# Kernel tuning notes

Measured on AMD Instinct MI355X. Metric: run time of the kernel, lower is better.

The kernel has to match this reference:

```python
import jax, jax.numpy as jnp
import numpy as np
from math import comb

# --- module hyperparameters (from init_kwargs / module-level constants) ---
F = 32          # features
NITER = 3       # num_iterations
NB = 16         # num_basis_functions
NDCM = 4        # n_dcm
CUTOFF = 4.0
MAXZ = 17       # max_atomic_number
NC = 9          # (max_degree+1)^2 spherical components, max_degree=2
DEG = np.array([0, 1, 1, 1, 2, 2, 2, 2, 2])  # degree l of each component
BINOM = jnp.asarray([comb(NB - 1, k) for k in range(NB)], dtype=jnp.float32)


def _np_sph9(x, y, z):
    # real spherical harmonics up to l=2 on the unit sphere (numpy, for Gaunt table)
    c0 = 0.28209479177387814; c1 = 0.4886025119029199
    c2a = 1.0925484305920792; c2b = 0.31539156525252005; c2c = 0.5462742152960396
    return np.stack([c0 * np.ones_like(x), c1 * y, c1 * z, c1 * x,
                     c2a * x * y, c2a * y * z, c2b * (3.0 * z * z - 1.0),
                     c2a * x * z, c2c * (x * x - y * y)], axis=0)


def _gaunt():
    # real Gaunt (Clebsch-Gordan-type) coefficients G[a,b,c] = int Y_a Y_b Y_c dOmega
    # via Gauss-Legendre (cos theta) x midpoint (phi) quadrature -- exact for l<=2 products
    ct, wt = np.polynomial.legendre.leggauss(64)
    nph = 256
    phi = (np.arange(nph) + 0.5) * (2.0 * np.pi / nph)
    st = np.sqrt(1.0 - ct ** 2)
    x = st[:, None] * np.cos(phi)[None, :]
    y = st[:, None] * np.sin(phi)[None, :]
    z = np.broadcast_to(ct[:, None], x.shape)
    w = (wt[:, None] * (2.0 * np.pi / nph)) * np.ones((1, nph))
    Y = _np_sph9(x, y, z)
    G = np.einsum('aij,bij,cij,ij->abc', Y, Y, Y, w)
    G[np.abs(G) < 1e-6] = 0.0
    return G

CG = jnp.asarray(_gaunt(), dtype=jnp.float32)  # (9, 9, 9), sparse


def _sph9(u):
    # u: (E, 3) unit vectors -> (E, 9)
    x, y, z = u[:, 0], u[:, 1], u[:, 2]
    c0 = 0.28209479177387814; c1 = 0.4886025119029199
    c2a = 1.0925484305920792; c2b = 0.31539156525252005; c2c = 0.5462742152960396
    return jnp.stack([jnp.full_like(x, c0), c1 * y, c1 * z, c1 * x,
                      c2a * x * y, c2a * y * z, c2b * (3.0 * z * z - 1.0),
                      c2a * x * z, c2c * (x * x - y * y)], axis=-1)


def _radial(r):
    # reciprocal Bernstein radial basis * smooth cutoff; r: (E,) -> (E, NB)
    u = 1.0 / (1.0 + r)
    k = jnp.arange(NB, dtype=jnp.float32)
    rb = BINOM * u[:, None] ** k * (1.0 - u[:, None]) ** (NB - 1 - k)
    t = r / CUTOFF
    den = jnp.where(t < 1.0, 1.0 - t * t, 1.0)
    fc = jnp.where(t < 1.0, jnp.exp(-t * t / den), 0.0)  # smooth_cutoff
    return rb * fc[:, None]


def _equiv_dense(x, W, b=None):
    # per-degree linear (equivariant Dense): x (N, 9, Fin), W (3, Fin, Fout); bias on l=0 only
    y = jnp.einsum('ncf,cfg->ncg', x, W[DEG])
    if b is not None:
        y = y.at[:, 0, :].add(b)
    return y


def _tp(xs, bf):
    # Gaunt tensor-product contraction: out[e,c,f] = sum_ab CG[a,b,c] xs[e,a,f] bf[e,b,f]
    # loop over the 9 fixed output components to avoid an (E,9,9,F) intermediate
    out = []
    for c in range(NC):
        t = jnp.einsum('eaf,ab->ebf', xs, CG[:, :, c])
        out.append(jnp.sum(t * bf, axis=1))
    return jnp.stack(out, axis=1)


def _forward(atomic_numbers, positions, dst_idx, src_idx, embed, Wb, W1, b1, W2, b2,
             Wt00, Wt11, Wmono, element_bias):
    n = atomic_numbers.shape[0]
    disp = positions[src_idx] - positions[dst_idx]                 # (E, 3) gather
    r = jnp.sqrt(jnp.sum(disp * disp, axis=-1) + 1e-12)            # safe norm
    u = disp / r[:, None]
    basis = _sph9(u)[:, :, None] * _radial(r)[:, None, :]          # (E, 9, NB)
    x = jnp.zeros((n, NC, F), dtype=positions.dtype).at[:, 0, :].set(embed[atomic_numbers])
    for i in range(NITER):  # message passing iterations
        bf = jnp.einsum('ebn,bng->ebg', basis, Wb[i][DEG])         # per-degree radial->feature mix (E,9,F)
        msg = _tp(x[src_idx], bf)                                  # gather src + tensor product
        y = x + jax.ops.segment_sum(msg, dst_idx, num_segments=n)  # scatter-aggregate + residual add
        y = _equiv_dense(y, W1[i], b1[i])
        y = jax.nn.silu(y)
        y = _equiv_dense(y, W2[i], b2[i])
        x = x + y                                                  # residual update
    # TensorDense to n_dcm channels, then readout heads
    mono = (x[:, 0, :] @ Wt00) @ Wmono + element_bias[atomic_numbers][:, None]  # (N, NDCM)
    dip = jnp.einsum('ncf,fg->ncg', x[:, 1:4, :], Wt11)            # (N, 3, NDCM) vector channel
    dip = jnp.clip(jax.nn.silu(dip), -0.3, 0.3) + positions[:, :, None]
    return mono, dip


def setup_inputs():
    key = jax.random.key(0)
    ks = jax.random.split(key, 12)
    N, E = 10000, 160000
    return {
        'atomic_numbers': jax.random.randint(ks[0], (N,), 0, MAXZ + 1),
        'positions': jax.random.normal(ks[1], (N, 3), jnp.float32) * 3.0,
        'dst_idx': jax.random.randint(ks[2], (E,), 0, N),
        'src_idx': jax.random.randint(ks[3], (E,), 0, N),
        'embed': jax.random.normal(ks[4], (MAXZ + 1, F), jnp.float32),
        'Wb': jax.random.normal(ks[5], (NITER, 3, NB, F), jnp.float32) / np.sqrt(NB).astype(np.float32),
        'W1': jax.random.normal(ks[6], (NITER, 3, F, F), jnp.float32) / np.sqrt(F).astype(np.float32),
        'b1': jnp.zeros((NITER, F), jnp.float32),
        'W2': jax.random.normal(ks[7], (NITER, 3, F, F), jnp.float32) / np.sqrt(F).astype(np.float32),
        'b2': jnp.zeros((NITER, F), jnp.float32),
        'Wt00': jax.random.normal(ks[8], (F, NDCM), jnp.float32) / np.sqrt(F).astype(np.float32),
        'Wt11': jax.random.normal(ks[9], (F, NDCM), jnp.float32) / np.sqrt(F).astype(np.float32),
        'Wmono': jax.random.normal(ks[10], (NDCM, NDCM), jnp.float32) / np.sqrt(NDCM).astype(np.float32),
        'element_bias': jnp.zeros((MAXZ + 1,), jnp.float32),
    }


def reference(atomic_numbers, positions, dst_idx, src_idx, embed, Wb, W1, b1, W2, b2,
              Wt00, Wt11, Wmono, element_bias):
    return _forward(atomic_numbers, positions, dst_idx, src_idx, embed, Wb, W1, b1, W2, b2,
                    Wt00, Wt11, Wmono, element_bias)
```

## Files before the change

kernel.cpp:

```cpp
#include <hip/hip_runtime.h>
#include <hip/hip_bf16.h>


#define NITER 3
#define BCAP  64

#define OFF_WB    0
#define OFF_W1    4608
#define OFF_B1    13824
#define OFF_W2    13920
#define OFF_B2    23136
#define OFF_WT00  23232
#define OFF_WT11  23360
#define OFF_WMONO 23488
#define OFF_EB    23504
#define OFF_EMB   23522
#define WC_TOTAL  24098

__device__ __forceinline__ float b2f(const __hip_bfloat16 v) { return __bfloat162float(v); }

#define KC0 0.28209479177387814f
#define KG1 0.21850968611841584f
#define KG2 0.12615662610100802f
#define KG3 0.18022375157287861f
#define KG4 0.09011187578643931f
#define KG5 0.15607834722743988f

__device__ __forceinline__ float ldany(const void* p, int i, bool f32) {
    return f32 ? ((const float*)p)[i] : b2f(((const __hip_bfloat16*)p)[i]);
}

__device__ __forceinline__ bool wave_sniff(const void* pos) {
    const __hip_bfloat16* p = (const __hip_bfloat16*)pos;
    int lane = threadIdx.x & 63;
    int bad = 0;
    #pragma unroll
    for (int k = 0; k < 4; k++) {
        float v = b2f(p[lane + k*64]);
        bad |= !(fabsf(v) < 1.0e6f);
    }
    return __ballot(bad) != 0ull;
}

__device__ __forceinline__ float xadd32(float v) {
    return v + __int_as_float(__shfl_xor(__float_as_int(v), 32, 64));
}

__device__ __forceinline__ bool edge_geom(float dx, float dy, float dz,
                                          float* sp, float* rad) {
    float r2 = dx*dx + dy*dy + dz*dz + 1e-12f;
    if (r2 >= 16.0f) return false;
    float r  = sqrtf(r2);
    float t2 = r2 * 0.0625f;
    float fc = __expf(-t2 / (1.0f - t2));
    float u = 1.0f / (1.0f + r);
    float v = 1.0f - u;
    const float BIN[16] = {1.f,15.f,105.f,455.f,1365.f,3003.f,5005.f,6435.f,
                           6435.f,5005.f,3003.f,1365.f,455.f,105.f,15.f,1.f};
    float vp[16];
    vp[0] = 1.0f;
    #pragma unroll
    for (int k = 1; k < 16; k++) vp[k] = vp[k-1] * v;
    float up = 1.0f;
    #pragma unroll
    for (int n = 0; n < 16; n++) { rad[n] = BIN[n] * up * vp[15-n] * fc; up *= u; }
    float ir = 1.0f / r;
    float ux = dx*ir, uy = dy*ir, uz = dz*ir;
    const float c0 = 0.28209479177387814f, c1 = 0.4886025119029199f;
    const float c2a = 1.0925484305920792f, c2b = 0.31539156525252005f, c2c = 0.5462742152960396f;
    sp[0] = c0;
    sp[1] = c1*uy; sp[2] = c1*uz; sp[3] = c1*ux;
    sp[4] = c2a*ux*uy; sp[5] = c2a*uy*uz; sp[6] = c2b*(3.0f*uz*uz - 1.0f);
    sp[7] = c2a*ux*uz; sp[8] = c2c*(ux*ux - uy*uy);
    return true;
}

__device__ __forceinline__ void write_geo_slot(float* gp,
                                               const float* sp, const float* rad) {
    float4* g4 = (float4*)gp;
    g4[0] = make_float4(sp[0], sp[1], sp[2], sp[3]);
    g4[1] = make_float4(sp[4], sp[5], sp[6], sp[7]);
    g4[2] = make_float4(sp[8], 0.f, 0.f, 0.f);
    g4[4] = make_float4(rad[0],  rad[1],  rad[2],  rad[3]);
    g4[5] = make_float4(rad[4],  rad[5],  rad[6],  rad[7]);
    g4[6] = make_float4(rad[8],  rad[9],  rad[10], rad[11]);
    g4[7] = make_float4(rad[12], rad[13], rad[14], rad[15]);
}

template <bool FIRST, bool LAST>
__global__ __launch_bounds__(256, 4) void iter_kernel(
        const float* __restrict__ xin, float* __restrict__ xout,
        const float* __restrict__ geo2, const int* __restrict__ cur,
        const int* __restrict__ sidx,
        const float* __restrict__ Wbi,
        const float* __restrict__ W1i, const float* __restrict__ b1i,
        const float* __restrict__ W2i, const float* __restrict__ b2i,
        const int* __restrict__ an, const float* __restrict__ posf,
        const float* __restrict__ wc, const void* __restrict__ pos,
        void* __restrict__ out_, int N) {
    constexpr int NCH = LAST ? 4 : 9;
    constexpr int NR  = LAST ? 2 : 5;
    __shared__ float sw[1536];
    __shared__ float sm[4][12][33];
    bool f32o = false;
    if (LAST) f32o = wave_sniff(pos);
    int tid   = threadIdx.x;
    int wslot = tid >> 6;
    int lane  = tid & 63;
    int f     = lane & 31;
    int half  = lane >> 5;
    int n     = blockIdx.x * 4 + wslot;
    bool act  = (n < N);
    float (*tile)[33] = sm[wslot];

    for (int i = tid; i < 1536; i += 256) sw[i] = Wbi[i];
    __syncthreads();

    float A0=0.f,A1=0.f,A2=0.f,A3=0.f,A4=0.f,A5=0.f,A6=0.f,A7=0.f,A8=0.f;
    if (act) {
        int cnt = __builtin_amdgcn_readfirstlane(cur[n]);
        int h0c = (cnt + 1) >> 1;
        int beg = n * BCAP;
        int b0  = beg + (half ? h0c : 0);
        int b1e = beg + (half ? cnt : h0c);
        int e = b0;
        int s_cur = (e < b1e) ? sidx[e] : 0;
        while (e < b1e) {
            int s_nxt = (e + 1 < b1e) ? sidx[e + 1] : 0;
            float X0, X1, X2, X3, X4, X5, X6, X7, X8;
            if (FIRST) {
                X0 = xin[(size_t)s_cur * 32 + f];
                X1=X2=X3=X4=X5=X6=X7=X8=0.f;
            } else {
                const float* xp = xin + (size_t)s_cur * 384 + f * 12;
                float4 xa = *(const float4*)(xp);
                float4 xb = *(const float4*)(xp + 4);
                X8 = xp[8];
                X0=xa.x; X1=xa.y; X2=xa.z; X3=xa.w;
                X4=xb.x; X5=xb.y; X6=xb.z; X7=xb.w;
            }
            const float4* gp = (const float4*)(geo2 + (size_t)e * 32);
            float4 h0 = gp[0], h1 = gp[1], h2 = gp[2];
            float4 r0 = gp[4], r1 = gp[5], r2 = gp[6], r3 = gp[7];
            float rad[16] = {r0.x,r0.y,r0.z,r0.w, r1.x,r1.y,r1.z,r1.w,
                             r2.x,r2.y,r2.z,r2.w, r3.x,r3.y,r3.z,r3.w};
            float rw0 = 0.f, rw1 = 0.f, rw2 = 0.f;
            #pragma unroll
            for (int k = 0; k < 16; k++) {
                rw0 = fmaf(rad[k], sw[       k*32 + f], rw0);
                rw1 = fmaf(rad[k], sw[ 512 + k*32 + f], rw1);
                rw2 = fmaf(rad[k], sw[1024 + k*32 + f], rw2);
            }
            float B0 = h0.x*rw0;
            float B1 = h0.y*rw1, B2 = h0.z*rw1, B3 = h0.w*rw1;
            float B4 = h1.x*rw2, B5 = h1.y*rw2, B6 = h1.z*rw2,
                  B7 = h1.w*rw2, B8 = h2.x*rw2;
            if (FIRST) {
                float k0 = KC0 * X0;
                A0 += k0*B0; A1 += k0*B1; A2 += k0*B2; A3 += k0*B3; A4 += k0*B4;
                A5 += k0*B5; A6 += k0*B6; A7 += k0*B7; A8 += k0*B8;
            } else {
                A0 += KC0*(X0*B0 + X1*B1 + X2*B2 + X3*B3 + X4*B4 + X5*B5 + X6*B6 + X7*B7 + X8*B8);
                A1 += KC0*(X0*B1 + X1*B0) + KG1*(X3*B4 + X4*B3 + X2*B5 + X5*B2)
                    - KG2*(X1*B6 + X6*B1) - KG1*(X1*B8 + X8*B1);
                A2 += KC0*(X0*B2 + X2*B0) + KG1*(X1*B5 + X5*B1 + X3*B7 + X7*B3)
                    + 2.0f*KG2*(X2*B6 + X6*B2);
                A3 += KC0*(X0*B3 + X3*B0) + KG1*(X1*B4 + X4*B1 + X2*B7 + X7*B2)
                    - KG2*(X3*B6 + X6*B3) + KG1*(X3*B8 + X8*B3);
                if (!LAST) {
                    A4 += KC0*(X0*B4 + X4*B0) + KG1*(X1*B3 + X3*B1) + KG5*(X5*B7 + X7*B5)
                        - KG3*(X4*B6 + X6*B4);
                    A5 += KC0*(X0*B5 + X5*B0) + KG1*(X1*B2 + X2*B1) + KG5*(X4*B7 + X7*B4)
                        + KG4*(X5*B6 + X6*B5) - KG5*(X5*B8 + X8*B5);
                    A6 += KC0*(X0*B6 + X6*B0) - KG2*X1*B1 + 2.0f*KG2*X2*B2 - KG2*X3*B3
                        - KG3*X4*B4 + KG4*X5*B5 + KG3*X6*B6 + KG4*X7*B7 - KG3*X8*B8;
                    A7 += KC0*(X0*B7 + X7*B0) + KG1*(X2*B3 + X3*B2) + KG5*(X4*B5 + X5*B4)
                        + KG4*(X6*B7 + X7*B6) + KG5*(X7*B8 + X8*B7);
                    A8 += KC0*(X0*B8 + X8*B0) - KG1*X1*B1 + KG1*X3*B3 - KG5*X5*B5 + KG5*X7*B7
                        - KG3*(X6*B8 + X8*B6);
                }
            }
            s_cur = s_nxt; e++;
        }
    }
    A0 = xadd32(A0); A1 = xadd32(A1); A2 = xadd32(A2); A3 = xadd32(A3);
    if (!LAST) {
        A4 = xadd32(A4); A5 = xadd32(A5); A6 = xadd32(A6);
        A7 = xadd32(A7); A8 = xadd32(A8);
    }

    float xr[9];
    #pragma unroll
    for (int c = 0; c < 9; c++) xr[c] = 0.f;
    if (act) {
        if (FIRST) {
            xr[0] = xin[(size_t)n * 32 + f];
        } else {
            const float* xp = xin + (size_t)n * 384 + f * 12;
            float4 xa = *(const float4*)(xp);
            float4 xb = *(const float4*)(xp + 4);
            xr[0]=xa.x; xr[1]=xa.y; xr[2]=xa.z; xr[3]=xa.w;
            xr[4]=xb.x; xr[5]=xb.y; xr[6]=xb.z; xr[7]=xb.w;
            xr[8]=xp[8];
        }
    }

    if (act && half == 0) {
        tile[0][f] = xr[0] + A0;
        tile[1][f] = xr[1] + A1;
        tile[2][f] = xr[2] + A2;
        tile[3][f] = xr[3] + A3;
        if (!LAST) {
            tile[4][f] = xr[4] + A4;
            tile[5][f] = xr[5] + A5;
            tile[6][f] = xr[6] + A6;
            tile[7][f] = xr[7] + A7;
            tile[8][f] = xr[8] + A8;
        }
    }
    __syncthreads();

    int g = f;
    float o1[NR];
    #pragma unroll
    for (int cc = 0; cc < NR; cc++) {
        int c  = cc*2 + half;
        int cs = (c < NCH) ? c : 0;
        int d  = (cs == 0) ? 0 : ((cs < 4) ? 1 : 2);
        const float* W1p = W1i + d * 1024;
        float acc = (c == 0) ? b1i[g] : 0.f;
        #pragma unroll
        for (int fi = 0; fi < 32; fi++)
            acc = fmaf(tile[cs][fi], W1p[fi*32 + g], acc);
        acc = acc * __builtin_amdgcn_rcpf(1.0f + __expf(-acc));
        o1[cc] = acc;
    }
    __syncthreads();
    #pragma unroll
    for (int cc = 0; cc < NR; cc++) {
        int c = cc*2 + half;
        if (c < NCH) tile[c][g] = o1[cc];
    }
    __syncthreads();

    float xf[NR];
    #pragma unroll
    for (int cc = 0; cc < NR; cc++) {
        int c  = cc*2 + half;
        int cs = (c < NCH) ? c : 0;
        int d  = (cs == 0) ? 0 : ((cs < 4) ? 1 : 2);
        const float* W2p = W2i + d * 1024;
        float acc = (c == 0) ? b2i[g] : 0.f;
        #pragma unroll
        for (int fi = 0; fi < 32; fi++)
            acc = fmaf(tile[cs][fi], W2p[fi*32 + g], acc);
        xf[cc] = xr[cs] + acc;
        if (LAST && act) {
            const float* WT = (c == 0) ? (wc + OFF_WT00) : (wc + OFF_WT11);
            float v0 = xf[cc] * WT[g*4 + 0];
            float v1 = xf[cc] * WT[g*4 + 1];
            float v2 = xf[cc] * WT[g*4 + 2];
            float v3 = xf[cc] * WT[g*4 + 3];
            #pragma unroll
            for (int m = 1; m <= 16; m <<= 1) {
                v0 += __shfl_xor(v0, m, 64);
                v1 += __shfl_xor(v1, m, 64);
                v2 += __shfl_xor(v2, m, 64);
                v3 += __shfl_xor(v3, m, 64);
            }
            if (g == 0) {
                if (c == 0) {
                    const float* Wmono = wc + OFF_WMONO;
                    float ebv = wc[OFF_EB + an[n]];
                    #pragma unroll
                    for (int m = 0; m < 4; m++) {
                        float a2 = ebv + v0*Wmono[0*4+m] + v1*Wmono[1*4+m]
                                       + v2*Wmono[2*4+m] + v3*Wmono[3*4+m];
                        if (f32o) ((float*)out_)[n*4 + m] = a2;
                        else ((__hip_bfloat16*)out_)[n*4 + m] = __float2bfloat16(a2);
                    }
                } else {
                    float pc = posf[n*3 + (c - 1)];
                    float pv[4] = {v0, v1, v2, v3};
                    #pragma unroll
                    for (int m = 0; m < 4; m++) {
                        float v = pv[m];
                        v = v * __builtin_amdgcn_rcpf(1.0f + __expf(-v));
                        v = fminf(fmaxf(v, -0.3f), 0.3f);
                        v += pc;
                        size_t o = (size_t)N*4 + (size_t)n*12 + (size_t)(c-1)*4 + m;
                        if (f32o) ((float*)out_)[o] = v;
                        else ((__hip_bfloat16*)out_)[o] = __float2bfloat16(v);
                    }
                }
            }
        }
    }
    if (!LAST) {
        __syncthreads();
        #pragma unroll
        for (int cc = 0; cc < NR; cc++) {
            int c = cc*2 + half;
            if (c < 9) tile[c][g] = xf[cc];
        }
        if (half == 1) { tile[9][g] = 0.f; tile[10][g] = 0.f; tile[11][g] = 0.f; }
        __syncthreads();
        if (act) {
            float* xo = xout + (size_t)n * 384;
            *(float4*)(xo + f*12 + half*4) =
                make_float4(tile[half*4+0][f], tile[half*4+1][f],
                            tile[half*4+2][f], tile[half*4+3][f]);
            if (half == 0)
                *(float4*)(xo + f*12 + 8) =
                    make_float4(tile[8][f], tile[9][f], tile[10][f], tile[11][f]);
        }
    }
}

__global__ void setup_kernel(const void* pos, const void* Wb, const void* W1,
        const void* b1, const void* W2, const void* b2, const void* Wt00,
        const void* Wt11, const void* Wmono, const void* eb, const void* emb,
        const int* __restrict__ an,
        const int* __restrict__ srcI, const int* __restrict__ dstI,
        float* __restrict__ posf, float* __restrict__ wc,
        float* __restrict__ x, float* __restrict__ geo2, int* __restrict__ cur,
        int* __restrict__ sidx, int N, int E, int use_csr) {
    bool f32 = wave_sniff(pos);
    int i = blockIdx.x * blockDim.x + threadIdx.x;
    int np = N * 3;
    if (i < np) { posf[i] = ldany(pos, i, f32); return; }
    int j = i - np;
    if (j < WC_TOTAL) {
        const void* src; int rel;
        if      (j < OFF_W1)    { src = Wb;    rel = j; }
        else if (j < OFF_B1)    { src = W1;    rel = j - OFF_W1; }
        else if (j < OFF_W2)    { src = b1;    rel = j - OFF_B1; }
        else if (j < OFF_B2)    { src = W2;    rel = j - OFF_W2; }
        else if (j < OFF_WT00)  { src = b2;    rel = j - OFF_B2; }
        else if (j < OFF_WT11)  { src = Wt00;  rel = j - OFF_WT00; }
        else if (j < OFF_WMONO) { src = Wt11;  rel = j - OFF_WT11; }
        else if (j < OFF_EB)    { src = Wmono; rel = j - OFF_WMONO; }
        else if (j < OFF_EMB)   { src = eb;    rel = j - OFF_EB; }
        else                    { src = emb;   rel = j - OFF_EMB; }
        wc[j] = ldany(src, rel, f32);
        return;
    }
    j -= WC_TOTAL;
    if (j < N * 32) {
        int n = j >> 5, rem = j & 31;
        size_t o = use_csr ? ((size_t)n * 32 + rem)
                           : ((size_t)n * 288 + rem);
        x[o] = ldany(emb, an[n] * 32 + rem, f32);
        return;
    }
    j -= N * 32;
    if (j < E && use_csr) {
        int s = srcI[j], d = dstI[j];
        float sp[9], rad[16];
        if (!edge_geom(ldany(pos, s*3+0, f32) - ldany(pos, d*3+0, f32),
                       ldany(pos, s*3+1, f32) - ldany(pos, d*3+1, f32),
                       ldany(pos, s*3+2, f32) - ldany(pos, d*3+2, f32),
                       sp, rad)) return;
        int slot = atomicAdd(&cur[d], 1);
        sidx[d * BCAP + slot] = s;
        write_geo_slot(geo2 + ((size_t)d * BCAP + slot) * 32, sp, rad);
    }
}

__global__ void zero_kernel(float4* __restrict__ b, int n) {
    int i = blockIdx.x * blockDim.x + threadIdx.x;
    int stride = gridDim.x * blockDim.x;
    float4 z = make_float4(0.f, 0.f, 0.f, 0.f);
    for (; i < n; i += stride) b[i] = z;
}

__global__ __launch_bounds__(256) void edge_inline_kernel(
        const float* __restrict__ x, float* __restrict__ y,
        const float* __restrict__ posf,
        const int* __restrict__ srcI, const int* __restrict__ dstI,
        const float* __restrict__ Wbi, int E) {
    int f  = threadIdx.x & 31;
    int hw = (blockIdx.x * blockDim.x + threadIdx.x) >> 5;
    int nhw = gridDim.x * (blockDim.x >> 5);
    float w0[16], w1[16], w2[16];
    #pragma unroll
    for (int n = 0; n < 16; n++) {
        w0[n] = Wbi[(0*16 + n)*32 + f];
        w1[n] = Wbi[(1*16 + n)*32 + f];
        w2[n] = Wbi[(2*16 + n)*32 + f];
    }
    for (int e = hw; e < E; e += nhw) {
        int s = srcI[e], d = dstI[e];
        float sp[9], rad[16];
        if (!edge_geom(posf[s*3+0] - posf[d*3+0],
                       posf[s*3+1] - posf[d*3+1],
                       posf[s*3+2] - posf[d*3+2], sp, rad)) continue;
        float rw0 = 0.f, rw1 = 0.f, rw2 = 0.f;
        #pragma unroll
        for (int n = 0; n < 16; n++) {
            rw0 = fmaf(rad[n], w0[n], rw0);
            rw1 = fmaf(rad[n], w1[n], rw1);
            rw2 = fmaf(rad[n], w2[n], rw2);
        }
        float B0 = sp[0]*rw0;
        float B1 = sp[1]*rw1, B2 = sp[2]*rw1, B3 = sp[3]*rw1;
        float B4 = sp[4]*rw2, B5 = sp[5]*rw2, B6 = sp[6]*rw2,
              B7 = sp[7]*rw2, B8 = sp[8]*rw2;
        const float* xp = x + (size_t)s*288 + f;
        float X0 = xp[0],   X1 = xp[32],  X2 = xp[64],  X3 = xp[96],  X4 = xp[128];
        float X5 = xp[160], X6 = xp[192], X7 = xp[224], X8 = xp[256];
        float* yp = y + (size_t)d*288 + f;
        float m;
        m = KC0*(X0*B0 + X1*B1 + X2*B2 + X3*B3 + X4*B4 + X5*B5 + X6*B6 + X7*B7 + X8*B8);
        unsafeAtomicAdd(yp + 0, m);
        m = KC0*(X0*B1 + X1*B0) + KG1*(X3*B4 + X4*B3 + X2*B5 + X5*B2)
          - KG2*(X1*B6 + X6*B1) - KG1*(X1*B8 + X8*B1);
        unsafeAtomicAdd(yp + 32, m);
        m = KC0*(X0*B2 + X2*B0) + KG1*(X1*B5 + X5*B1 + X3*B7 + X7*B3)
          + 2.0f*KG2*(X2*B6 + X6*B2);
        unsafeAtomicAdd(yp + 64, m);
        m = KC0*(X0*B3 + X3*B0) + KG1*(X1*B4 + X4*B1 + X2*B7 + X7*B2)
          - KG2*(X3*B6 + X6*B3) + KG1*(X3*B8 + X8*B3);
        unsafeAtomicAdd(yp + 96, m);
        m = KC0*(X0*B4 + X4*B0) + KG1*(X1*B3 + X3*B1) + KG5*(X5*B7 + X7*B5)
          - KG3*(X4*B6 + X6*B4);
        unsafeAtomicAdd(yp + 128, m);
        m = KC0*(X0*B5 + X5*B0) + KG1*(X1*B2 + X2*B1) + KG5*(X4*B7 + X7*B4)
          + KG4*(X5*B6 + X6*B5) - KG5*(X5*B8 + X8*B5);
        unsafeAtomicAdd(yp + 160, m);
        m = KC0*(X0*B6 + X6*B0) - KG2*X1*B1 + 2.0f*KG2*X2*B2 - KG2*X3*B3
          - KG3*X4*B4 + KG4*X5*B5 + KG3*X6*B6 + KG4*X7*B7 - KG3*X8*B8;
        unsafeAtomicAdd(yp + 192, m);
        m = KC0*(X0*B7 + X7*B0) + KG1*(X2*B3 + X3*B2) + KG5*(X4*B5 + X5*B4)
          + KG4*(X6*B7 + X7*B6) + KG5*(X7*B8 + X8*B7);
        unsafeAtomicAdd(yp + 224, m);
        m = KC0*(X0*B8 + X8*B0) - KG1*X1*B1 + KG1*X3*B3 - KG5*X5*B5 + KG5*X7*B7
          - KG3*(X6*B8 + X8*B6);
        unsafeAtomicAdd(yp + 256, m);
    }
}

__global__ __launch_bounds__(256) void atom_kernel(
        float* __restrict__ x, const float* __restrict__ y,
        const float* __restrict__ W1i, const float* __restrict__ b1i,
        const float* __restrict__ W2i, const float* __restrict__ b2i,
        int N) {
    __shared__ float sm[4][64*33];
    int lane  = threadIdx.x & 63;
    int wslot = threadIdx.x >> 6;
    int u = __builtin_amdgcn_readfirstlane(blockIdx.x * 4 + wslot);
    int t = u / 9;
    int c = u - t * 9;
    int d = (c == 0) ? 0 : ((c < 4) ? 1 : 2);
    const float* W1 = W1i + d * 1024;
    const float* W2 = W2i + d * 1024;
    float* tile = sm[wslot];
    float4 xr4[8];
    #pragma unroll
    for (int k = 0; k < 8; k++) {
        int e  = lane * 4 + k * 256;
        int al = e >> 5, f = e & 31;
        int ag = t * 64 + al;
        float4 s = make_float4(0.f, 0.f, 0.f, 0.f);
        float4 xv = make_float4(0.f, 0.f, 0.f, 0.f);
        if (ag < N) {
            xv = *(const float4*)(x + (size_t)ag * 288 + c * 32 + f);
            float4 yv = *(const float4*)(y + (size_t)ag * 288 + c * 32 + f);
            s = make_float4(xv.x + yv.x, xv.y + yv.y, xv.z + yv.z, xv.w + yv.w);
        }
        xr4[k] = xv;
        *(float4*)(tile + al * 33 + f) = s;
    }
    __syncthreads();
    float yin[32];
    #pragma unroll
    for (int k = 0; k < 8; k++) {
        float4 v = *(const float4*)(tile + lane * 33 + 4 * k);
        yin[4*k+0] = v.x; yin[4*k+1] = v.y; yin[4*k+2] = v.z; yin[4*k+3] = v.w;
    }
    float acc[32];
    #pragma unroll
    for (int g = 0; g < 32; g++) acc[g] = (c == 0) ? b1i[g] : 0.0f;
    #pragma unroll 4
    for (int fi = 0; fi < 32; fi++) {
        float v = yin[fi];
        #pragma unroll
        for (int g = 0; g < 32; g++) acc[g] = fmaf(v, W1[fi*32 + g], acc[g]);
    }
    #pragma unroll
    for (int g = 0; g < 32; g++)
        acc[g] = acc[g] * __builtin_amdgcn_rcpf(1.0f + __expf(-acc[g]));
    float out[32];
    #pragma unroll
    for (int g = 0; g < 32; g++) out[g] = (c == 0) ? b2i[g] : 0.0f;
    #pragma unroll 4
    for (int fi = 0; fi < 32; fi++) {
        float v = acc[fi];
        #pragma unroll
        for (int g = 0; g < 32; g++) out[g] = fmaf(v, W2[fi*32 + g], out[g]);
    }
    __syncthreads();
    #pragma unroll
    for (int k = 0; k < 8; k++)
        *(float4*)(tile + lane * 33 + 4 * k) =
            make_float4(out[4*k+0], out[4*k+1], out[4*k+2], out[4*k+3]);
    __syncthreads();
    #pragma unroll
    for (int k = 0; k < 8; k++) {
        int e  = lane * 4 + k * 256;
        int al = e >> 5, f = e & 31;
        int ag = t * 64 + al;
        if (ag < N) {
            float4 dv = *(const float4*)(tile + al * 33 + f);
            float4 xv = xr4[k];
            *(float4*)(x + (size_t)ag * 288 + c * 32 + f) =
                make_float4(xv.x + dv.x, xv.y + dv.y, xv.z + dv.z, xv.w + dv.w);
        }
    }
}

__global__ void readout_kernel(const float* __restrict__ x,
        const int* __restrict__ an, const float* __restrict__ posf,
        const float* __restrict__ wc, const void* __restrict__ pos,
        void* __restrict__ out, int N) {
    bool f32 = wave_sniff(pos);
    int n = blockIdx.x * blockDim.x + threadIdx.x;
    if (n >= N) return;
    const float* Wt00  = wc + OFF_WT00;
    const float* Wt11  = wc + OFF_WT11;
    const float* Wmono = wc + OFF_WMONO;
    const float* xb = x + (size_t)n * 288;
    float q[4] = {0.f, 0.f, 0.f, 0.f};
    for (int f = 0; f < 32; f++) {
        float xv = xb[f];
        #pragma unroll
        for (int j = 0; j < 4; j++) q[j] = fmaf(xv, Wt00[f*4 + j], q[j]);
    }
    float ebv = wc[OFF_EB + an[n]];
    #pragma unroll
    for (int m = 0; m < 4; m++) {
        float acc = ebv;
        #pragma unroll
        for (int j = 0; j < 4; j++) acc = fmaf(q[j], Wmono[j*4 + m], acc);
        if (f32) ((float*)out)[n*4 + m] = acc;
        else ((__hip_bfloat16*)out)[n*4 + m] = __float2bfloat16(acc);
    }
    #pragma unroll
    for (int c = 0; c < 3; c++) {
        float pc = posf[n*3 + c];
        const float* xc = xb + (1 + c)*32;
        float dq[4] = {0.f, 0.f, 0.f, 0.f};
        for (int f = 0; f < 32; f++) {
            float xv = xc[f];
            #pragma unroll
            for (int m = 0; m < 4; m++) dq[m] = fmaf(xv, Wt11[f*4 + m], dq[m]);
        }
        #pragma unroll
        for (int m = 0; m < 4; m++) {
            float v = dq[m];
            v = v * __builtin_amdgcn_rcpf(1.0f + __expf(-v));
            v = fminf(fmaxf(v, -0.3f), 0.3f);
            v += pc;
            if (f32) ((float*)out)[N*4 + n*12 + c*4 + m] = v;
            else ((__hip_bfloat16*)out)[N*4 + n*12 + c*4 + m] = __float2bfloat16(v);
        }
    }
}

extern "C" void kernel_launch(void* const* d_in, const int* in_sizes, int n_in,
                              void* d_out, int out_size, void* d_ws, size_t ws_size,
                              hipStream_t stream) {
    const int* an    = (const int*)d_in[0];
    const void* pos  = d_in[1];
    const int* dstI  = (const int*)d_in[2];
    const int* srcI  = (const int*)d_in[3];
    const void* embed= d_in[4];
    const void* Wb   = d_in[5];
    const void* W1   = d_in[6];
    const void* b1   = d_in[7];
    const void* W2   = d_in[8];
    const void* b2   = d_in[9];
    const void* Wt00 = d_in[10];
    const void* Wt11 = d_in[11];
    const void* Wmono= d_in[12];
    const void* eb   = d_in[13];
    int N = in_sizes[0];
    int E = in_sizes[2];

    {
        float* x0c  = (float*)d_ws;
        float* x1   = x0c + (size_t)N * 32;
        float* x2   = x1 + (size_t)N * 384;
        float* posf = x2 + (size_t)N * 384;
        float* wc   = posf + (size_t)N * 3;
        int* cur    = (int*)(wc + WC_TOTAL);
        int* sidx   = cur + N;
        uintptr_t ga = ((uintptr_t)(sidx + (size_t)N * BCAP) + 127) & ~(uintptr_t)127;
        float* geo2 = (float*)ga;
        size_t need = (uintptr_t)(geo2 + (size_t)N * BCAP * 32) - (uintptr_t)d_ws;
        if (ws_size >= need) {
            hipMemsetAsync(cur, 0, sizeof(int) * (size_t)N, stream);
            int tot = N * 3 + WC_TOTAL + N * 32 + E;
            setup_kernel<<<(tot + 255)/256, 256, 0, stream>>>(
                pos, Wb, W1, b1, W2, b2, Wt00, Wt11, Wmono, eb, embed,
                an, srcI, dstI, posf, wc, x0c, geo2, cur, sidx, N, E, 1);
            int gblocks = (N + 3) / 4;
            iter_kernel<true,false><<<gblocks, 256, 0, stream>>>(
                x0c, x1, geo2, cur, sidx,
                wc + OFF_WB, wc + OFF_W1, wc + OFF_B1, wc + OFF_W2, wc + OFF_B2,
                an, posf, wc, pos, d_out, N);
            iter_kernel<false,false><<<gblocks, 256, 0, stream>>>(
                x1, x2, geo2, cur, sidx,
                wc + OFF_WB + 1536, wc + OFF_W1 + 3072, wc + OFF_B1 + 32,
                wc + OFF_W2 + 3072, wc + OFF_B2 + 32,
                an, posf, wc, pos, d_out, N);
            iter_kernel<false,true><<<gblocks, 256, 0, stream>>>(
                x2, nullptr, geo2, cur, sidx,
                wc + OFF_WB + 3072, wc + OFF_W1 + 6144, wc + OFF_B1 + 64,
                wc + OFF_W2 + 6144, wc + OFF_B2 + 64,
                an, posf, wc, pos, d_out, N);
            return;
        }
    }

    float* x    = (float*)d_ws;
    float* y    = x + (size_t)N * 288;
    float* posf = y + (size_t)N * 288;
    float* wc   = posf + (size_t)N * 3;
    int* cur    = (int*)(wc + WC_TOTAL);
    int ntiles = (N + 63) / 64;

    hipMemsetAsync(cur, 0, sizeof(int) * (size_t)N, stream);
    zero_kernel<<<512, 256, 0, stream>>>((float4*)x, N * 72);
    {
        int tot = N * 3 + WC_TOTAL + N * 32;
        setup_kernel<<<(tot + 255)/256, 256, 0, stream>>>(
            pos, Wb, W1, b1, W2, b2, Wt00, Wt11, Wmono, eb, embed,
            an, srcI, dstI, posf, wc, x, nullptr, cur, nullptr, N, E, 0);
    }
    int ablocks = (ntiles * 9 + 3) / 4;
    for (int i = 0; i < NITER; i++) {
        zero_kernel<<<512, 256, 0, stream>>>((float4*)y, N * 72);
        edge_inline_kernel<<<2048, 256, 0, stream>>>(x, y, posf, srcI, dstI,
            wc + OFF_WB + (size_t)i*1536, E);
        atom_kernel<<<ablocks, 256, 0, stream>>>(x, y,
            wc + OFF_W1 + (size_t)i*3072, wc + OFF_B1 + (size_t)i*32,
            wc + OFF_W2 + (size_t)i*3072, wc + OFF_B2 + (size_t)i*32, N);
    }
    readout_kernel<<<(N + 255)/256, 256, 0, stream>>>(x, an, posf, wc, pos,
                                                      d_out, N);
}
```

Baseline: 236.4 us.

## Switch node features to channel-major layout and interleave edges across half-waves

Node features move from an interleaved [N][32][12] layout to channel-major [9][N][32], so each gather reads 32 contiguous floats per channel and the output is written directly without staging through shared memory. The two half-waves now take alternating edges instead of contiguous halves, and the next source node's features are prefetched into registers before the current edge is computed. This aims to cut uncoalesced strided gathers, padding traffic and an extra shared-memory round trip with its barriers. In exchange there are more load instructions per edge and higher register pressure from the prefetch buffer.

```diff
diff --git a/kernel.cpp b/kernel.cpp
--- a/kernel.cpp
+++ b/kernel.cpp
@@ -97,11 +97,11 @@
         const float* __restrict__ W2i, const float* __restrict__ b2i,
         const int* __restrict__ an, const float* __restrict__ posf,
         const float* __restrict__ wc, const void* __restrict__ pos,
-        void* __restrict__ out_, int N) {
+        void* __restrict__ out_, int N, int NS) {
     constexpr int NCH = LAST ? 4 : 9;
     constexpr int NR  = LAST ? 2 : 5;
     __shared__ float sw[1536];
-    __shared__ float sm[4][12][33];
+    __shared__ float sm[4][9][33];
     bool f32o = false;
     if (LAST) f32o = wave_sniff(pos);
     int tid   = threadIdx.x;
@@ -119,25 +119,26 @@
     float A0=0.f,A1=0.f,A2=0.f,A3=0.f,A4=0.f,A5=0.f,A6=0.f,A7=0.f,A8=0.f;
     if (act) {
         int cnt = __builtin_amdgcn_readfirstlane(cur[n]);
-        int h0c = (cnt + 1) >> 1;
         int beg = n * BCAP;
-        int b0  = beg + (half ? h0c : 0);
-        int b1e = beg + (half ? cnt : h0c);
-        int e = b0;
-        int s_cur = (e < b1e) ? sidx[e] : 0;
-        while (e < b1e) {
-            int s_nxt = (e + 1 < b1e) ? sidx[e + 1] : 0;
-            float X0, X1, X2, X3, X4, X5, X6, X7, X8;
+        int eend = beg + cnt;
+        int e = beg + half;
+        int s_cur = (e < eend) ? sidx[e] : 0;
+        float Xc[9];
+        if (FIRST) {
+            Xc[0] = xin[s_cur * 32 + f];
+        } else {
+            #pragma unroll
+            for (int c = 0; c < 9; c++) Xc[c] = xin[c*NS + s_cur*32 + f];
+        }
+        while (e < eend) {
+            int e2 = e + 2;
+            int s_nxt = (e2 < eend) ? sidx[e2] : 0;
+            float Xn[9];
             if (FIRST) {
-                X0 = xin[(size_t)s_cur * 32 + f];
-                X1=X2=X3=X4=X5=X6=X7=X8=0.f;
+                Xn[0] = xin[s_nxt * 32 + f];
             } else {
-                const float* xp = xin + (size_t)s_cur * 384 + f * 12;
-                float4 xa = *(const float4*)(xp);
-                float4 xb = *(const float4*)(xp + 4);
-                X8 = xp[8];
-                X0=xa.x; X1=xa.y; X2=xa.z; X3=xa.w;
-                X4=xb.x; X5=xb.y; X6=xb.z; X7=xb.w;
+                #pragma unroll
+                for (int c = 0; c < 9; c++) Xn[c] = xin[c*NS + s_nxt*32 + f];
             }
             const float4* gp = (const float4*)(geo2 + (size_t)e * 32);
             float4 h0 = gp[0], h1 = gp[1], h2 = gp[2];
@@ -156,10 +157,12 @@
             float B4 = h1.x*rw2, B5 = h1.y*rw2, B6 = h1.z*rw2,
                   B7 = h1.w*rw2, B8 = h2.x*rw2;
             if (FIRST) {
-                float k0 = KC0 * X0;
+                float k0 = KC0 * Xc[0];
                 A0 += k0*B0; A1 += k0*B1; A2 += k0*B2; A3 += k0*B3; A4 += k0*B4;
                 A5 += k0*B5; A6 += k0*B6; A7 += k0*B7; A8 += k0*B8;
             } else {
+                float X0=Xc[0],X1=Xc[1],X2=Xc[2],X3=Xc[3],X4=Xc[4],
+                      X5=Xc[5],X6=Xc[6],X7=Xc[7],X8=Xc[8];
                 A0 += KC0*(X0*B0 + X1*B1 + X2*B2 + X3*B3 + X4*B4 + X5*B5 + X6*B6 + X7*B7 + X8*B8);
                 A1 += KC0*(X0*B1 + X1*B0) + KG1*(X3*B4 + X4*B3 + X2*B5 + X5*B2)
                     - KG2*(X1*B6 + X6*B1) - KG1*(X1*B8 + X8*B1);
@@ -180,7 +183,9 @@
                         - KG3*(X6*B8 + X8*B6);
                 }
             }
-            s_cur = s_nxt; e++;
+            #pragma unroll
+            for (int c = 0; c < 9; c++) Xc[c] = Xn[c];
+            e = e2; s_cur = s_nxt;
         }
     }
     A0 = xadd32(A0); A1 = xadd32(A1); A2 = xadd32(A2); A3 = xadd32(A3);
@@ -194,14 +199,10 @@
     for (int c = 0; c < 9; c++) xr[c] = 0.f;
     if (act) {
         if (FIRST) {
-            xr[0] = xin[(size_t)n * 32 + f];
+            xr[0] = xin[n * 32 + f];
         } else {
-            const float* xp = xin + (size_t)n * 384 + f * 12;
-            float4 xa = *(const float4*)(xp);
-            float4 xb = *(const float4*)(xp + 4);
-            xr[0]=xa.x; xr[1]=xa.y; xr[2]=xa.z; xr[3]=xa.w;
-            xr[4]=xb.x; xr[5]=xb.y; xr[6]=xb.z; xr[7]=xb.w;
-            xr[8]=xp[8];
+            #pragma unroll
+            for (int c = 0; c < NCH; c++) xr[c] = xin[c*NS + n*32 + f];
         }
     }
 
@@ -243,7 +244,6 @@
     }
     __syncthreads();
 
-    float xf[NR];
     #pragma unroll
     for (int cc = 0; cc < NR; cc++) {
         int c  = cc*2 + half;
@@ -254,13 +254,16 @@
         #pragma unroll
         for (int fi = 0; fi < 32; fi++)
             acc = fmaf(tile[cs][fi], W2p[fi*32 + g], acc);
-        xf[cc] = xr[cs] + acc;
-        if (LAST && act) {
+        float xf = xr[cs] + acc;
+        if (!LAST) {
+            if (act && c < 9)
+                xout[c*NS + n*32 + g] = xf;
+        } else if (act) {
             const float* WT = (c == 0) ? (wc + OFF_WT00) : (wc + OFF_WT11);
-            float v0 = xf[cc] * WT[g*4 + 0];
-            float v1 = xf[cc] * WT[g*4 + 1];
-            float v2 = xf[cc] * WT[g*4 + 2];
-            float v3 = xf[cc] * WT[g*4 + 3];
+            float v0 = xf * WT[g*4 + 0];
+            float v1 = xf * WT[g*4 + 1];
+            float v2 = xf * WT[g*4 + 2];
+            float v3 = xf * WT[g*4 + 3];
             #pragma unroll
             for (int m = 1; m <= 16; m <<= 1) {
                 v0 += __shfl_xor(v0, m, 64);
@@ -294,25 +297,6 @@
                     }
                 }
             }
-        }
-    }
-    if (!LAST) {
-        __syncthreads();
-        #pragma unroll
-        for (int cc = 0; cc < NR; cc++) {
-            int c = cc*2 + half;
-            if (c < 9) tile[c][g] = xf[cc];
-        }
-        if (half == 1) { tile[9][g] = 0.f; tile[10][g] = 0.f; tile[11][g] = 0.f; }
-        __syncthreads();
-        if (act) {
-            float* xo = xout + (size_t)n * 384;
-            *(float4*)(xo + f*12 + half*4) =
-                make_float4(tile[half*4+0][f], tile[half*4+1][f],
-                            tile[half*4+2][f], tile[half*4+3][f]);
-            if (half == 0)
-                *(float4*)(xo + f*12 + 8) =
-                    make_float4(tile[8][f], tile[9][f], tile[10][f], tile[11][f]);
         }
     }
 }
@@ -586,12 +570,13 @@
     const void* eb   = d_in[13];
     int N = in_sizes[0];
     int E = in_sizes[2];
+    int NS = N * 32;
 
     {
         float* x0c  = (float*)d_ws;
         float* x1   = x0c + (size_t)N * 32;
-        float* x2   = x1 + (size_t)N * 384;
-        float* posf = x2 + (size_t)N * 384;
+        float* x2   = x1 + (size_t)N * 288;
+        float* posf = x2 + (size_t)N * 288;
         float* wc   = posf + (size_t)N * 3;
         int* cur    = (int*)(wc + WC_TOTAL);
         int* sidx   = cur + N;
@@ -608,17 +593,17 @@
             iter_kernel<true,false><<<gblocks, 256, 0, stream>>>(
                 x0c, x1, geo2, cur, sidx,
                 wc + OFF_WB, wc + OFF_W1, wc + OFF_B1, wc + OFF_W2, wc + OFF_B2,
-                an, posf, wc, pos, d_out, N);
+                an, posf, wc, pos, d_out, N, NS);
             iter_kernel<false,false><<<gblocks, 256, 0, stream>>>(
                 x1, x2, geo2, cur, sidx,
                 wc + OFF_WB + 1536, wc + OFF_W1 + 3072, wc + OFF_B1 + 32,
                 wc + OFF_W2 + 3072, wc + OFF_B2 + 32,
-                an, posf, wc, pos, d_out, N);
+                an, posf, wc, pos, d_out, N, NS);
             iter_kernel<false,true><<<gblocks, 256, 0, stream>>>(
                 x2, nullptr, geo2, cur, sidx,
                 wc + OFF_WB + 3072, wc + OFF_W1 + 6144, wc + OFF_B1 + 64,
                 wc + OFF_W2 + 6144, wc + OFF_B2 + 64,
-                an, posf, wc, pos, d_out, N);
+                an, posf, wc, pos, d_out, N, NS);
             return;
         }
     }
```

Measured after the change: 223.1 us. 5.6% less time.
